# Performance work log

Measured on AMD Instinct MI355X. Metric: run time of the kernel, lower is better.

The kernel has to match this reference:

```python
import jax, jax.numpy as jnp
import numpy as np

N, F, H, FO = 4096, 512, 4, 128  # nodes, in-feat, heads, out-feat per head
NEG_INF = -1e10
LRELU_ALPHA = 0.2


def setup_inputs() -> dict:
    key = jax.random.key(0)
    k_x, k_a, k_w, k_as, k_an = jax.random.split(key, 5)
    X = jax.random.normal(k_x, (N, F), dtype=jnp.float32)
    A = (jax.random.uniform(k_a, (N, N)) < 0.01).astype(jnp.float32)
    A = jnp.minimum(A + jnp.eye(N, dtype=jnp.float32), 1.0)
    W = jax.random.normal(k_w, (H, F, FO), dtype=jnp.float32) * 0.05       # per-head kernels
    b = jnp.zeros((H, FO), dtype=jnp.float32)                               # per-head biases
    a_self = jax.random.normal(k_as, (H, FO), dtype=jnp.float32) * 0.05    # attn_kernel_self (F_,1) per head
    a_neigh = jax.random.normal(k_an, (H, FO), dtype=jnp.float32) * 0.05   # attn_kernel_neigh (F_,1) per head
    return {"X": X, "A": A, "W": W, "b": b, "a_self": a_self, "a_neigh": a_neigh}


def reference(X, A, W, b, a_self, a_neigh):
    # features[h] = X @ W[h] -> [H, N, FO]
    feats = jnp.einsum('nf,hfo->hno', X, W)
    # Nx1 self / neighbor scores per head -> [H, N]
    e_s = jnp.einsum('hno,ho->hn', feats, a_self)
    e_n = jnp.einsum('hno,ho->hn', feats, a_neigh)
    # broadcast-add to [H, N, N], LeakyReLU(0.2), additive adjacency mask
    logits = e_s[:, :, None] + e_n[:, None, :]
    logits = jnp.where(logits > 0, logits, LRELU_ALPHA * logits)
    logits = logits + NEG_INF * (1.0 - A)[None, :, :]
    attn = jax.nn.softmax(logits, axis=-1)          # [H, N, N]
    out = jnp.einsum('hnm,hmo->hno', attn, feats)   # weighted aggregate
    out = out + b[:, None, :]
    # concat heads: [N, H*FO]
    out = jnp.transpose(out, (1, 0, 2)).reshape(X.shape[0], -1)
    return jax.nn.relu(out)
```

## Files before the change

### kernel.cpp

```cpp
#include <hip/hip_runtime.h>
#include <math.h>

#define NODES 4096
#define FIN   512
#define HEADS 4
#define FOUT  128
#define COLS  512
#define MAXNBR 128

typedef _Float16 half8   __attribute__((ext_vector_type(8)));
typedef float    floatx4 __attribute__((ext_vector_type(4)));
typedef float    floatx2 __attribute__((ext_vector_type(2)));
typedef unsigned int uint4v __attribute__((ext_vector_type(4)));

__global__ __launch_bounds__(256) void gemm_scan(
    const float* __restrict__ X, const float* __restrict__ W,
    const float* __restrict__ A,
    const float* __restrict__ a_self, const float* __restrict__ a_neigh,
    _Float16* __restrict__ feats_h, float* __restrict__ e_s, float* __restrict__ e_n,
    unsigned int* __restrict__ nbr_pack, int* __restrict__ nbr_cnt)
{
    const int tid = threadIdx.x;

    if (blockIdx.x >= 512) {
        __shared__ int            cnt4[4];
        __shared__ unsigned short idx4[4][MAXNBR];
        const int w = tid >> 6, lane = tid & 63;
        const int row = (blockIdx.x - 512) * 4 + w;
        if (lane == 0) cnt4[w] = 0;
        const uint4v* Arow = (const uint4v*)(A + (size_t)row * NODES);
        for (int q = lane; q < NODES / 4; q += 64) {
            uint4v v = __builtin_nontemporal_load(Arow + q);
            int j = q * 4;
            if (v[0]) { int p = atomicAdd(&cnt4[w], 1); if (p < MAXNBR) idx4[w][p] = (unsigned short)j; }
            if (v[1]) { int p = atomicAdd(&cnt4[w], 1); if (p < MAXNBR) idx4[w][p] = (unsigned short)(j + 1); }
            if (v[2]) { int p = atomicAdd(&cnt4[w], 1); if (p < MAXNBR) idx4[w][p] = (unsigned short)(j + 2); }
            if (v[3]) { int p = atomicAdd(&cnt4[w], 1); if (p < MAXNBR) idx4[w][p] = (unsigned short)(j + 3); }
        }
        __syncthreads();
        unsigned int packed = ((unsigned int)idx4[w][2 * lane + 1] << 16) | idx4[w][2 * lane];
        nbr_pack[(size_t)row * 64 + lane] = packed;
        if (lane == 0) nbr_cnt[row] = min(cnt4[w], MAXNBR);
        return;
    }

    __shared__ _Float16 Ah[2][64][40];
    __shared__ _Float16 Bh[2][64][40];
    const int rowBase = (blockIdx.x >> 3) * 64;
    const int colBase = (blockIdx.x & 7) * 64;
    const int h     = colBase >> 7;
    const int obase = colBase & 127;
    const int lane = tid & 63, w = tid >> 6;
    const int quad = lane >> 4, lk = quad * 8, lm = lane & 15;

    const int sr = tid >> 2, sk = (tid & 3) * 8;
    const float* xp = X + (size_t)(rowBase + sr) * FIN + sk;
    const int o = tid & 63, fg = tid >> 6;
    const float* wp = W + ((size_t)h * FIN + fg * 8) * FOUT + obase + o;

    floatx4 acc[4];
    #pragma unroll
    for (int mi = 0; mi < 4; mi++) acc[mi] = (floatx4)0.f;

    float4 xa = *(const float4*)(xp);
    float4 xb = *(const float4*)(xp + 4);
    float rw[8];
    #pragma unroll
    for (int ii = 0; ii < 8; ii++) rw[ii] = wp[(size_t)ii * FOUT];

    for (int it = 0; it < FIN / 32; ++it) {
        const int cur = it & 1;
        half8 ha, hb;
        ha[0] = (_Float16)xa.x; ha[1] = (_Float16)xa.y;
        ha[2] = (_Float16)xa.z; ha[3] = (_Float16)xa.w;
        ha[4] = (_Float16)xb.x; ha[5] = (_Float16)xb.y;
        ha[6] = (_Float16)xb.z; ha[7] = (_Float16)xb.w;
        #pragma unroll
        for (int ii = 0; ii < 8; ii++) hb[ii] = (_Float16)rw[ii];
        *(half8*)&Ah[cur][sr][sk]    = ha;
        *(half8*)&Bh[cur][o][fg * 8] = hb;
        if (it + 1 < FIN / 32) {
            int k0 = (it + 1) * 32;
            xa = *(const float4*)(xp + k0);
            xb = *(const float4*)(xp + k0 + 4);
            #pragma unroll
            for (int ii = 0; ii < 8; ii++) rw[ii] = wp[(size_t)(k0 + ii) * FOUT];
        }
        __syncthreads();
        half8 bfrag = *(const half8*)&Bh[cur][w * 16 + lm][lk];
        #pragma unroll
        for (int mi = 0; mi < 4; mi++) {
            half8 afrag = *(const half8*)&Ah[cur][mi * 16 + lm][lk];
            acc[mi] = __builtin_amdgcn_mfma_f32_16x16x32_f16(afrag, bfrag, acc[mi], 0, 0, 0);
        }
    }

    const int col = colBase + w * 16 + lm;
    const float as = a_self[col], an = a_neigh[col];
    #pragma unroll
    for (int mi = 0; mi < 4; mi++) {
        #pragma unroll
        for (int r = 0; r < 4; r++) {
            int row = rowBase + mi * 16 + quad * 4 + r;
            float v = acc[mi][r];
            feats_h[(size_t)row * COLS + col] = (_Float16)v;
            float vs = v * as, vn = v * an;
            #pragma unroll
            for (int off = 1; off < 16; off <<= 1) {
                vs += __shfl_xor(vs, off, 64);
                vn += __shfl_xor(vn, off, 64);
            }
            if (lm == 0) {
                atomicAdd(&e_s[h * NODES + row], vs);
                atomicAdd(&e_n[h * NODES + row], vn);
            }
        }
    }
}

__global__ __launch_bounds__(256) void aggregate(
    const _Float16* __restrict__ feats_h,
    const float* __restrict__ e_s, const float* __restrict__ e_n,
    const unsigned int* __restrict__ nbr_pack, const int* __restrict__ nbr_cnt,
    const float* __restrict__ bias, float* __restrict__ out)
{
    const int i = blockIdx.x;
    const int tid = threadIdx.x;
    __shared__ unsigned short s_idx[MAXNBR];
    __shared__ float s_w[HEADS][MAXNBR];
    __shared__ float s_part[HEADS][520];
    __shared__ float s_dinv[HEADS];

    const int cnt = nbr_cnt[i];
    if (tid < 64) {
        unsigned v = nbr_pack[(size_t)i * 64 + tid];
        s_idx[2 * tid]     = (unsigned short)(v & 0xFFFF);
        s_idx[2 * tid + 1] = (unsigned short)(v >> 16);
    }
    __syncthreads();

    const int wv = tid >> 6, lane = tid & 63;
    const float esi = e_s[wv * NODES + i];
    const float* enh = e_n + wv * NODES;

    float m = -1e30f;
    for (int k = lane; k < cnt; k += 64) {
        float e = esi + enh[s_idx[k]];
        m = fmaxf(m, e > 0.f ? e : 0.2f * e);
    }
    #pragma unroll
    for (int off = 32; off > 0; off >>= 1) m = fmaxf(m, __shfl_xor(m, off, 64));

    float d = 0.f;
    for (int k = lane; k < cnt; k += 64) {
        float e = esi + enh[s_idx[k]];
        float l = e > 0.f ? e : 0.2f * e;
        float wgt = __expf(l - m);
        s_w[wv][k] = wgt;
        d += wgt;
    }
    #pragma unroll
    for (int off = 32; off > 0; off >>= 1) d += __shfl_xor(d, off, 64);
    if (lane == 0) s_dinv[wv] = 1.f / d;
    __syncthreads();

    float acc[8];
    #pragma unroll
    for (int u = 0; u < 8; u++) acc[u] = 0.f;
    const int hl = lane >> 4;
    const _Float16* fcol = feats_h + lane * 8;

    for (int k0 = wv; k0 < cnt; k0 += 16) {
        int idx[4]; float wt[4];
        #pragma unroll
        for (int u = 0; u < 4; u++) {
            int k = k0 + u * 4;
            bool vld = (k < cnt);
            int kc = vld ? k : k0;
            idx[u] = s_idx[kc];
            wt[u]  = vld ? s_w[hl][kc] : 0.f;
        }
        half8 f[4];
        #pragma unroll
        for (int u = 0; u < 4; u++)
            f[u] = *(const half8*)(fcol + (size_t)idx[u] * COLS);
        #pragma unroll
        for (int u = 0; u < 4; u++)
            #pragma unroll
            for (int e8 = 0; e8 < 8; e8++)
                acc[e8] = fmaf(wt[u], (float)f[u][e8], acc[e8]);
    }

    *(floatx4*)&s_part[wv][lane * 8]     = *(floatx4*)&acc[0];
    *(floatx4*)&s_part[wv][lane * 8 + 4] = *(floatx4*)&acc[4];
    __syncthreads();

    const int c = 2 * tid;
    const int h = c >> 7;
    float o0 = s_part[0][c]     + s_part[1][c]     + s_part[2][c]     + s_part[3][c];
    float o1 = s_part[0][c + 1] + s_part[1][c + 1] + s_part[2][c + 1] + s_part[3][c + 1];
    const float dinv = s_dinv[h];
    o0 = fmaxf(o0 * dinv + bias[c],     0.f);
    o1 = fmaxf(o1 * dinv + bias[c + 1], 0.f);
    floatx2 res; res[0] = o0; res[1] = o1;
    __builtin_nontemporal_store(res, (floatx2*)(out + (size_t)i * COLS + c));
}

extern "C" void kernel_launch(void* const* d_in, const int* in_sizes, int n_in,
                              void* d_out, int out_size, void* d_ws, size_t ws_size,
                              hipStream_t stream) {
    const float* X       = (const float*)d_in[0];
    const float* A       = (const float*)d_in[1];
    const float* W       = (const float*)d_in[2];
    const float* b       = (const float*)d_in[3];
    const float* a_self  = (const float*)d_in[4];
    const float* a_neigh = (const float*)d_in[5];
    float* out = (float*)d_out;

    _Float16*     feats_h  = (_Float16*)d_ws;
    float*        e_s      = (float*)(feats_h + (size_t)NODES * COLS);
    float*        e_n      = e_s + HEADS * NODES;
    unsigned int* nbr_pack = (unsigned int*)(e_n + HEADS * NODES);
    int*          nbr_cnt  = (int*)(nbr_pack + (size_t)NODES * 64);

    hipMemsetAsync(e_s, 0, 2 * HEADS * NODES * sizeof(float), stream);
    gemm_scan<<<1536, 256, 0, stream>>>(X, W, A, a_self, a_neigh,
                                        feats_h, e_s, e_n, nbr_pack, nbr_cnt);
    aggregate<<<NODES, 256, 0, stream>>>(feats_h, e_s, e_n, nbr_pack, nbr_cnt, b, out);
}
```

Measured before the change: 147.5 us.

## Replace score atomics with partial slots and restructure aggregation per head-wave

The GEMM kernel now reduces the attention-score partials in shared memory and writes them to per-half slots, replacing global atomics. That also removes the memset before the launch. The aggregate kernel gives each wave one head: it sums the two partial slots, skips the softmax max-subtraction pass, and accumulates two columns per lane, so the cross-wave shared-memory reduction and block barriers disappear. Skipping the max shift risks exp overflow if attention logits are large, and the narrower half2 gathers mean more load instructions per neighbour.

```diff
diff --git a/kernel.cpp b/kernel.cpp
--- a/kernel.cpp
+++ b/kernel.cpp
@@ -9,6 +9,7 @@
 #define MAXNBR 128
 
 typedef _Float16 half8   __attribute__((ext_vector_type(8)));
+typedef _Float16 half2v  __attribute__((ext_vector_type(2)));
 typedef float    floatx4 __attribute__((ext_vector_type(4)));
 typedef float    floatx2 __attribute__((ext_vector_type(2)));
 typedef unsigned int uint4v __attribute__((ext_vector_type(4)));
@@ -17,7 +18,7 @@
     const float* __restrict__ X, const float* __restrict__ W,
     const float* __restrict__ A,
     const float* __restrict__ a_self, const float* __restrict__ a_neigh,
-    _Float16* __restrict__ feats_h, float* __restrict__ e_s, float* __restrict__ e_n,
+    _Float16* __restrict__ feats_h, float* __restrict__ ep_s, float* __restrict__ ep_n,
     unsigned int* __restrict__ nbr_pack, int* __restrict__ nbr_cnt)
 {
     const int tid = threadIdx.x;
@@ -46,9 +47,11 @@
 
     __shared__ _Float16 Ah[2][64][40];
     __shared__ _Float16 Bh[2][64][40];
+    __shared__ float red_s[4][64], red_n[4][64];
     const int rowBase = (blockIdx.x >> 3) * 64;
     const int colBase = (blockIdx.x & 7) * 64;
     const int h     = colBase >> 7;
+    const int half  = (colBase >> 6) & 1;
     const int obase = colBase & 127;
     const int lane = tid & 63, w = tid >> 6;
     const int quad = lane >> 4, lk = quad * 8, lm = lane & 15;
@@ -101,107 +104,90 @@
     for (int mi = 0; mi < 4; mi++) {
         #pragma unroll
         for (int r = 0; r < 4; r++) {
-            int row = rowBase + mi * 16 + quad * 4 + r;
+            int lrow = mi * 16 + quad * 4 + r;
             float v = acc[mi][r];
-            feats_h[(size_t)row * COLS + col] = (_Float16)v;
+            feats_h[(size_t)(rowBase + lrow) * COLS + col] = (_Float16)v;
             float vs = v * as, vn = v * an;
             #pragma unroll
             for (int off = 1; off < 16; off <<= 1) {
                 vs += __shfl_xor(vs, off, 64);
                 vn += __shfl_xor(vn, off, 64);
             }
-            if (lm == 0) {
-                atomicAdd(&e_s[h * NODES + row], vs);
-                atomicAdd(&e_n[h * NODES + row], vn);
-            }
-        }
+            if (lm == 0) { red_s[w][lrow] = vs; red_n[w][lrow] = vn; }
+        }
+    }
+    __syncthreads();
+    if (tid < 64) {
+        float vs = red_s[0][tid] + red_s[1][tid] + red_s[2][tid] + red_s[3][tid];
+        float vn = red_n[0][tid] + red_n[1][tid] + red_n[2][tid] + red_n[3][tid];
+        size_t slot = (size_t)(half * HEADS + h) * NODES + rowBase + tid;
+        ep_s[slot] = vs;
+        ep_n[slot] = vn;
     }
 }
 
 __global__ __launch_bounds__(256) void aggregate(
     const _Float16* __restrict__ feats_h,
-    const float* __restrict__ e_s, const float* __restrict__ e_n,
+    const float* __restrict__ ep_s, const float* __restrict__ ep_n,
     const unsigned int* __restrict__ nbr_pack, const int* __restrict__ nbr_cnt,
     const float* __restrict__ bias, float* __restrict__ out)
 {
     const int i = blockIdx.x;
     const int tid = threadIdx.x;
+    const int wv = tid >> 6, lane = tid & 63;
     __shared__ unsigned short s_idx[MAXNBR];
     __shared__ float s_w[HEADS][MAXNBR];
-    __shared__ float s_part[HEADS][520];
-    __shared__ float s_dinv[HEADS];
 
     const int cnt = nbr_cnt[i];
-    if (tid < 64) {
-        unsigned v = nbr_pack[(size_t)i * 64 + tid];
-        s_idx[2 * tid]     = (unsigned short)(v & 0xFFFF);
-        s_idx[2 * tid + 1] = (unsigned short)(v >> 16);
-    }
-    __syncthreads();
-
-    const int wv = tid >> 6, lane = tid & 63;
-    const float esi = e_s[wv * NODES + i];
-    const float* enh = e_n + wv * NODES;
-
-    float m = -1e30f;
-    for (int k = lane; k < cnt; k += 64) {
-        float e = esi + enh[s_idx[k]];
-        m = fmaxf(m, e > 0.f ? e : 0.2f * e);
-    }
-    #pragma unroll
-    for (int off = 32; off > 0; off >>= 1) m = fmaxf(m, __shfl_xor(m, off, 64));
+    {
+        unsigned v = nbr_pack[(size_t)i * 64 + lane];
+        s_idx[2 * lane]     = (unsigned short)(v & 0xFFFF);
+        s_idx[2 * lane + 1] = (unsigned short)(v >> 16);
+    }
+
+    const float esi = ep_s[wv * NODES + i] + ep_s[(HEADS + wv) * NODES + i];
+    const float* en0 = ep_n + wv * NODES;
+    const float* en1 = ep_n + (HEADS + wv) * NODES;
 
     float d = 0.f;
     for (int k = lane; k < cnt; k += 64) {
-        float e = esi + enh[s_idx[k]];
+        int j = s_idx[k];
+        float e = esi + en0[j] + en1[j];
         float l = e > 0.f ? e : 0.2f * e;
-        float wgt = __expf(l - m);
+        float wgt = __expf(l);
         s_w[wv][k] = wgt;
         d += wgt;
     }
     #pragma unroll
     for (int off = 32; off > 0; off >>= 1) d += __shfl_xor(d, off, 64);
-    if (lane == 0) s_dinv[wv] = 1.f / d;
-    __syncthreads();
-
-    float acc[8];
-    #pragma unroll
-    for (int u = 0; u < 8; u++) acc[u] = 0.f;
-    const int hl = lane >> 4;
-    const _Float16* fcol = feats_h + lane * 8;
-
-    for (int k0 = wv; k0 < cnt; k0 += 16) {
-        int idx[4]; float wt[4];
-        #pragma unroll
-        for (int u = 0; u < 4; u++) {
-            int k = k0 + u * 4;
+    const float dinv = 1.f / d;
+
+    float acc0 = 0.f, acc1 = 0.f;
+    const _Float16* fcol = feats_h + wv * FOUT + 2 * lane;
+    for (int k0 = 0; k0 < cnt; k0 += 8) {
+        int j8[8]; float w8[8];
+        #pragma unroll
+        for (int u = 0; u < 8; u++) {
+            int k = k0 + u;
             bool vld = (k < cnt);
             int kc = vld ? k : k0;
-            idx[u] = s_idx[kc];
-            wt[u]  = vld ? s_w[hl][kc] : 0.f;
-        }
-        half8 f[4];
-        #pragma unroll
-        for (int u = 0; u < 4; u++)
-            f[u] = *(const half8*)(fcol + (size_t)idx[u] * COLS);
-        #pragma unroll
-        for (int u = 0; u < 4; u++)
-            #pragma unroll
-            for (int e8 = 0; e8 < 8; e8++)
-                acc[e8] = fmaf(wt[u], (float)f[u][e8], acc[e8]);
-    }
-
-    *(floatx4*)&s_part[wv][lane * 8]     = *(floatx4*)&acc[0];
-    *(floatx4*)&s_part[wv][lane * 8 + 4] = *(floatx4*)&acc[4];
-    __syncthreads();
-
-    const int c = 2 * tid;
-    const int h = c >> 7;
-    float o0 = s_part[0][c]     + s_part[1][c]     + s_part[2][c]     + s_part[3][c];
-    float o1 = s_part[0][c + 1] + s_part[1][c + 1] + s_part[2][c + 1] + s_part[3][c + 1];
-    const float dinv = s_dinv[h];
-    o0 = fmaxf(o0 * dinv + bias[c],     0.f);
-    o1 = fmaxf(o1 * dinv + bias[c + 1], 0.f);
+            j8[u] = s_idx[kc];
+            w8[u] = vld ? s_w[wv][kc] : 0.f;
+        }
+        half2v f8[8];
+        #pragma unroll
+        for (int u = 0; u < 8; u++)
+            f8[u] = *(const half2v*)(fcol + (size_t)j8[u] * COLS);
+        #pragma unroll
+        for (int u = 0; u < 8; u++) {
+            acc0 = fmaf(w8[u], (float)f8[u][0], acc0);
+            acc1 = fmaf(w8[u], (float)f8[u][1], acc1);
+        }
+    }
+
+    const int c = wv * FOUT + 2 * lane;
+    float o0 = fmaxf(acc0 * dinv + bias[c],     0.f);
+    float o1 = fmaxf(acc1 * dinv + bias[c + 1], 0.f);
     floatx2 res; res[0] = o0; res[1] = o1;
     __builtin_nontemporal_store(res, (floatx2*)(out + (size_t)i * COLS + c));
 }
@@ -218,13 +204,12 @@
     float* out = (float*)d_out;
 
     _Float16*     feats_h  = (_Float16*)d_ws;
-    float*        e_s      = (float*)(feats_h + (size_t)NODES * COLS);
-    float*        e_n      = e_s + HEADS * NODES;
-    unsigned int* nbr_pack = (unsigned int*)(e_n + HEADS * NODES);
+    float*        ep_s     = (float*)(feats_h + (size_t)NODES * COLS);
+    float*        ep_n     = ep_s + 2 * HEADS * NODES;
+    unsigned int* nbr_pack = (unsigned int*)(ep_n + 2 * HEADS * NODES);
     int*          nbr_cnt  = (int*)(nbr_pack + (size_t)NODES * 64);
 
-    hipMemsetAsync(e_s, 0, 2 * HEADS * NODES * sizeof(float), stream);
     gemm_scan<<<1536, 256, 0, stream>>>(X, W, A, a_self, a_neigh,
-                                        feats_h, e_s, e_n, nbr_pack, nbr_cnt);
-    aggregate<<<NODES, 256, 0, stream>>>(feats_h, e_s, e_n, nbr_pack, nbr_cnt, b, out);
+                                        feats_h, ep_s, ep_n, nbr_pack, nbr_cnt);
+    aggregate<<<NODES, 256, 0, stream>>>(feats_h, ep_s, ep_n, nbr_pack, nbr_cnt, b, out);
 }
```

Result: no change. 145.2 us (-1.6%).
